# Kernel tuning notes

Measured on AMD Instinct MI355X. Metric: run time of the kernel, lower is better.

Reference implementation:

```python
import jax, jax.numpy as jnp
import numpy as np

A, M, H = 4, 1024, 1024
E, N = 8, 4096

def setup_inputs() -> dict:
    key = jax.random.key(0)
    kx, k1, k2 = jax.random.split(key, 3)
    x = jax.random.normal(kx, (A, M, H), dtype=jnp.float32)
    w1 = jax.random.normal(k1, (E, H, N), dtype=jnp.float32) * 0.02
    w2 = jax.random.normal(k2, (E, N, H), dtype=jnp.float32) * 0.02
    return {"x": x, "w1": w1, "w2": w2}

def reference(x, w1, w2):
    # mid: [A, E, M, N] = up-projection per expert
    mid = jnp.einsum('amh,ehn->aemn', x, w1)
    # down-projection per expert, then sum over experts e
    out = jnp.einsum('aemn,enh->amh', mid, w2)
    return out
```

## Files before the change

### kernel.cpp

```cpp
#include <hip/hip_runtime.h>
#include <hip/hip_bf16.h>
#include <stdint.h>


#define BN 128

typedef __attribute__((ext_vector_type(8))) short short8;
typedef __attribute__((ext_vector_type(4))) float float4v;
typedef __attribute__((ext_vector_type(4))) unsigned int uint4v;

__device__ __forceinline__ unsigned int rne_hi(unsigned int u) {
  return u + 0x7fffu + ((u >> 16) & 1u);
}

__device__ __forceinline__ unsigned int pack_bf16(float lo, float hi) {
  unsigned int ulo = rne_hi(__float_as_uint(lo));
  unsigned int uhi = rne_hi(__float_as_uint(hi));
  return __builtin_amdgcn_perm(uhi, ulo, 0x07060302u);
}

__device__ __forceinline__ void load_lds_16B(const void* g, void* lds) {
  __builtin_amdgcn_global_load_lds(
      (__attribute__((address_space(1))) void*)(uintptr_t)g,
      (__attribute__((address_space(3))) void*)(unsigned int)(uintptr_t)lds,
      16, 0, 0);
}

template <int MI, bool ATOMIC>
__global__ __launch_bounds__(256) void gemm_bf16(
    const unsigned short* __restrict__ A, int lda, long strideA,
    const unsigned short* __restrict__ Bt, int ldb, long strideB,
    float* __restrict__ C, int ldc, int K, int zdiv) {
  constexpr int BM = MI * 32;
  __shared__ __attribute__((aligned(16))) unsigned short As[2 * BM * 32];
  __shared__ __attribute__((aligned(16))) unsigned short Bs[2 * BN * 32];

  const int tid = threadIdx.x;
  const int wv = tid >> 6;
  const int ln = tid & 63;
  const int wm = (wv >> 1) * (MI * 16);
  const int wn = (wv & 1) * 64;
  const int lrow = ln & 15;
  const int lq = ln >> 4;
  const int sfrag = ((lq + (lrow >> 1)) & 3) * 16;

  const int zb = blockIdx.z / zdiv;
  const int zk = blockIdx.z % zdiv;
  const unsigned short* Ab = A + (long)zb * strideA + (long)zk * K +
                             (long)(blockIdx.y * BM) * lda;
  const unsigned short* Bb = Bt + (long)zb * strideB + (long)zk * K +
                             (long)(blockIdx.x * BN) * ldb;

  float4v zero4 = {0.0f, 0.0f, 0.0f, 0.0f};
  float4v acc[MI][4];
#pragma unroll
  for (int i = 0; i < MI; ++i)
#pragma unroll
    for (int j = 0; j < 4; ++j) acc[i][j] = zero4;

  const int nk = K / 64;
  for (int kt = 0; kt < nk; ++kt) {
    const int k0 = kt * 64;
    __syncthreads();
#pragma unroll
    for (int s = 0; s < 2; ++s) {
#pragma unroll
      for (int p = 0; p < BM / 64; ++p) {
        int o = p * 256 + wv * 64 + ln;
        int r = o >> 2;
        int gk = ((o & 3) - (r >> 1)) & 3;
        const unsigned short* g = Ab + (long)r * lda + k0 + s * 32 + gk * 8;
        char* lp = (char*)As + s * (BM * 64) + (p * 256 + wv * 64) * 16;
        load_lds_16B(g, lp);
      }
#pragma unroll
      for (int p = 0; p < 2; ++p) {
        int o = p * 256 + wv * 64 + ln;
        int r = o >> 2;
        int gk = ((o & 3) - (r >> 1)) & 3;
        const unsigned short* g = Bb + (long)r * ldb + k0 + s * 32 + gk * 8;
        char* lp = (char*)Bs + s * (BN * 64) + (p * 256 + wv * 64) * 16;
        load_lds_16B(g, lp);
      }
    }
    __syncthreads();

#pragma unroll
    for (int s = 0; s < 2; ++s) {
      short8 a[MI], b[4];
#pragma unroll
      for (int i = 0; i < MI; ++i)
        a[i] = *(const short8*)((const char*)As + s * (BM * 64) +
                                (wm + i * 16 + lrow) * 64 + sfrag);
#pragma unroll
      for (int j = 0; j < 4; ++j)
        b[j] = *(const short8*)((const char*)Bs + s * (BN * 64) +
                                (wn + j * 16 + lrow) * 64 + sfrag);
#pragma unroll
      for (int i = 0; i < MI; ++i)
#pragma unroll
        for (int j = 0; j < 4; ++j)
          acc[i][j] =
              __builtin_amdgcn_mfma_f32_16x16x32_bf16(a[i], b[j], acc[i][j], 0, 0, 0);
    }
  }

  const int crow0 = blockIdx.y * BM + wm + lq * 4;
  const int ccol0 = blockIdx.x * BN + wn + lrow;
#pragma unroll
  for (int i = 0; i < MI; ++i)
#pragma unroll
    for (int j = 0; j < 4; ++j)
#pragma unroll
      for (int r = 0; r < 4; ++r) {
        int row = crow0 + i * 16 + r;
        int col = ccol0 + j * 16;
        if (ATOMIC)
          atomicAdd(&C[(long)row * ldc + col], acc[i][j][r]);
        else
          C[(long)row * ldc + col] = acc[i][j][r];
      }
}

__global__ __launch_bounds__(256) void cvt_f32_bf16(
    const float* __restrict__ in, unsigned short* __restrict__ out) {
  long i = ((long)blockIdx.x * 256 + threadIdx.x) * 8;
  float4 v0 = *(const float4*)(in + i);
  float4 v1 = *(const float4*)(in + i + 4);
  uint4v d;
  d.x = pack_bf16(v0.x, v0.y);
  d.y = pack_bf16(v0.z, v0.w);
  d.z = pack_bf16(v1.x, v1.y);
  d.w = pack_bf16(v1.z, v1.w);
  *(uint4v*)(out + i) = d;
}

__global__ __launch_bounds__(256) void transpose_cvt_kernel(
    const float* __restrict__ in, unsigned short* __restrict__ out,
    int R, int C, long strideBatch) {
  __shared__ float tile[64][65];
  const float* src = in + (long)blockIdx.z * strideBatch;
  unsigned short* dst = out + (long)blockIdx.z * strideBatch;
  const int t = threadIdx.x;
  const int c4 = (t & 15) * 4;
  const int r0 = t >> 4;
  const int by = blockIdx.y * 64;
  const int bx = blockIdx.x * 64;
#pragma unroll
  for (int p = 0; p < 4; ++p) {
    int r = r0 + p * 16;
    float4 v = *(const float4*)(src + (long)(by + r) * C + bx + c4);
    tile[r][c4 + 0] = v.x;
    tile[r][c4 + 1] = v.y;
    tile[r][c4 + 2] = v.z;
    tile[r][c4 + 3] = v.w;
  }
  __syncthreads();
#pragma unroll
  for (int p = 0; p < 4; ++p) {
    int cc = r0 + p * 16;
    int rr = c4;
    unsigned int d0 = pack_bf16(tile[rr + 0][cc], tile[rr + 1][cc]);
    unsigned int d1 = pack_bf16(tile[rr + 2][cc], tile[rr + 3][cc]);
    uint2 dd;
    dd.x = d0;
    dd.y = d1;
    *(uint2*)(dst + (long)(bx + cc) * R + by + rr) = dd;
  }
}

extern "C" void kernel_launch(void* const* d_in, const int* in_sizes, int n_in,
                              void* d_out, int out_size, void* d_ws, size_t ws_size,
                              hipStream_t stream) {
  const float* x = (const float*)d_in[0];
  const float* w1 = (const float*)d_in[1];
  const float* w2 = (const float*)d_in[2];
  float* out = (float*)d_out;

  const int A_ = 4, M_ = 1024, H_ = 1024, E_ = 8, N_ = 4096;
  const long EXP = (long)H_ * N_;

  const size_t need_single =
      (size_t)2 * E_ * EXP * 2 + (size_t)A_ * M_ * H_ * 2 +
      (size_t)H_ * H_ * 4 + (size_t)H_ * H_ * 2;

  if (ws_size >= need_single) {
    unsigned short* w2t = (unsigned short*)d_ws;
    unsigned short* w1b = w2t + (long)E_ * EXP;
    unsigned short* xb = w1b + (long)E_ * EXP;
    float* Wacc = (float*)(xb + (long)A_ * M_ * H_);
    unsigned short* Wb = (unsigned short*)(Wacc + (long)H_ * H_);

    cvt_f32_bf16<<<(A_ * M_ * H_) / 2048, 256, 0, stream>>>(x, xb);
    transpose_cvt_kernel<<<dim3(H_ / 64, N_ / 64, E_), 256, 0, stream>>>(
        w2, w2t, N_, H_, EXP);
    cvt_f32_bf16<<<(int)(E_ * EXP / 2048), 256, 0, stream>>>(w1, w1b);
    hipMemsetAsync(Wacc, 0, (size_t)H_ * H_ * 4, stream);

    gemm_bf16<4, true><<<dim3(H_ / BN, H_ / 128, E_ * 2), 256, 0, stream>>>(
        w2t, N_, EXP, w1b, N_, EXP, Wacc, H_, N_ / 2, 2);

    cvt_f32_bf16<<<(H_ * H_) / 2048, 256, 0, stream>>>(Wacc, Wb);

    gemm_bf16<2, false><<<dim3(H_ / BN, (A_ * M_) / 64, 1), 256, 0, stream>>>(
        xb, H_, 0, Wb, H_, 0, out, H_, H_, 1);
  } else {
    unsigned short* w2t = (unsigned short*)d_ws;
    unsigned short* w1b = w2t + 4 * EXP;
    unsigned short* xb = w1b + 4 * EXP;
    float* Wacc = (float*)(xb + (long)A_ * M_ * H_);
    unsigned short* Wb = (unsigned short*)(Wacc + (long)H_ * H_);

    cvt_f32_bf16<<<(A_ * M_ * H_) / 2048, 256, 0, stream>>>(x, xb);
    hipMemsetAsync(Wacc, 0, (size_t)H_ * H_ * 4, stream);

    for (int g = 0; g < 2; ++g) {
      const float* w2g = w2 + (long)g * 4 * EXP;
      const float* w1g = w1 + (long)g * 4 * EXP;
      transpose_cvt_kernel<<<dim3(H_ / 64, N_ / 64, 4), 256, 0, stream>>>(
          w2g, w2t, N_, H_, EXP);
      cvt_f32_bf16<<<(int)(4 * EXP / 2048), 256, 0, stream>>>(w1g, w1b);
      gemm_bf16<4, true><<<dim3(H_ / BN, H_ / 128, 4 * 2), 256, 0, stream>>>(
          w2t, N_, EXP, w1b, N_, EXP, Wacc, H_, N_ / 2, 2);
    }

    cvt_f32_bf16<<<(H_ * H_) / 2048, 256, 0, stream>>>(Wacc, Wb);
    gemm_bf16<2, false><<<dim3(H_ / BN, (A_ * M_) / 64, 1), 256, 0, stream>>>(
        xb, H_, 0, Wb, H_, 0, out, H_, H_, 1);
  }
}
```

Measured before the change: 470.0 us.

## Replace weight-product GEMM with 256x256 tiled, 8-wave phased pipelined kernel

Adds a new GEMM for the W2^T·W1 weight-combination step. It uses 256x256 tiles with 512 threads, double-buffered LDS with an XOR swizzle, and a four-phase schedule per k-tile that interleaves global-to-LDS staging with MFMA groups run at raised wave priority. It also remaps workgroups across XCDs. The goal is to raise MFMA utilisation and data reuse over the old 128x128 kernel, at the cost of heavier register and LDS use and more barriers. In the fallback path the K split changes to 4 with grid 256.

```diff
diff --git a/kernel.cpp b/kernel.cpp
--- a/kernel.cpp
+++ b/kernel.cpp
@@ -24,6 +24,167 @@
       (__attribute__((address_space(1))) void*)(uintptr_t)g,
       (__attribute__((address_space(3))) void*)(unsigned int)(uintptr_t)lds,
       16, 0, 0);
+}
+
+
+template <int MH, int NH>
+__device__ __forceinline__ void mma_ph(float4v acc[8][4], const short8* aR,
+                                       const short8 bR[2][4]) {
+  __builtin_amdgcn_s_setprio(1);
+#pragma unroll
+  for (int fi = 0; fi < 4; ++fi)
+#pragma unroll
+    for (int fj = 0; fj < 2; ++fj)
+#pragma unroll
+      for (int s = 0; s < 2; ++s)
+        acc[MH * 4 + fi][NH * 2 + fj] = __builtin_amdgcn_mfma_f32_16x16x32_bf16(
+            aR[fi * 2 + s], bR[NH][fj * 2 + s], acc[MH * 4 + fi][NH * 2 + fj],
+            0, 0, 0);
+  __builtin_amdgcn_s_setprio(0);
+}
+
+__global__ __launch_bounds__(512, 2) void gemm1_8ph(
+    const unsigned short* __restrict__ A, const unsigned short* __restrict__ Bt,
+    float* __restrict__ C, long expStride, int ld, int Kc, int zdiv) {
+  __shared__ __attribute__((aligned(16))) unsigned short As[2][2][128 * 64];
+  __shared__ __attribute__((aligned(16))) unsigned short Bs[2][2][128 * 64];
+
+  const int tid = threadIdx.x;
+  const int wv = tid >> 6;
+  const int ln = tid & 63;
+  const int lrow = ln & 15;
+  const int lq = ln >> 4;
+  const int wmh = wv >> 2;
+  const int wnq = wv & 3;
+  const int breg = wnq >> 1;
+  const int brow0 = (wnq & 1) * 64;
+
+  const int nwg = gridDim.x;
+  int wg = blockIdx.x;
+  if ((nwg & 7) == 0) wg = (wg & 7) * (nwg >> 3) + (wg >> 3);
+  const int tile = wg & 15;
+  const int z = wg >> 4;
+  const int e = z / zdiv;
+  const int kc = z % zdiv;
+  const int ty = tile >> 2, tx = tile & 3;
+
+  const unsigned short* Ab =
+      A + (long)e * expStride + (long)(ty * 256) * ld + (long)kc * Kc;
+  const unsigned short* Bb =
+      Bt + (long)e * expStride + (long)(tx * 256) * ld + (long)kc * Kc;
+
+  const int srow = ln >> 3;
+  const int scg = (ln & 7) ^ srow;
+
+  auto stageA = [&](int b, int h, int kt) {
+#pragma unroll
+    for (int i = 0; i < 2; ++i) {
+      const unsigned short* g =
+          Ab + (long)(h * 128 + wv * 16 + i * 8 + srow) * ld + kt * 64 + scg * 8;
+      load_lds_16B(g, (void*)&As[b][h][(wv * 2 + i) * 512]);
+    }
+  };
+  auto stageB = [&](int b, int h, int kt) {
+#pragma unroll
+    for (int i = 0; i < 2; ++i) {
+      const unsigned short* g =
+          Bb + (long)(h * 128 + wv * 16 + i * 8 + srow) * ld + kt * 64 + scg * 8;
+      load_lds_16B(g, (void*)&Bs[b][h][(wv * 2 + i) * 512]);
+    }
+  };
+
+  float4v acc[8][4];
+  float4v zero4 = {0.0f, 0.0f, 0.0f, 0.0f};
+#pragma unroll
+  for (int i = 0; i < 8; ++i)
+#pragma unroll
+    for (int j = 0; j < 4; ++j) acc[i][j] = zero4;
+
+  short8 aR[8];
+  short8 bR[2][4];
+
+  auto ldsA = [&](int b, int mh) {
+#pragma unroll
+    for (int fi = 0; fi < 4; ++fi) {
+      const int row = mh * 64 + fi * 16 + lrow;
+#pragma unroll
+      for (int s = 0; s < 2; ++s) {
+        const int cg = (s * 4 + lq) ^ (row & 7);
+        aR[fi * 2 + s] = *(const short8*)&As[b][wmh][row * 64 + cg * 8];
+      }
+    }
+  };
+  auto ldsB = [&](int b, int nh) {
+#pragma unroll
+    for (int fj = 0; fj < 2; ++fj) {
+      const int row = brow0 + nh * 32 + fj * 16 + lrow;
+#pragma unroll
+      for (int s = 0; s < 2; ++s) {
+        const int cg = (s * 4 + lq) ^ (row & 7);
+        bR[nh][fj * 2 + s] = *(const short8*)&Bs[b][breg][row * 64 + cg * 8];
+      }
+    }
+  };
+
+  const int nkt = Kc / 64;
+
+  stageA(0, 0, 0);
+  stageA(0, 1, 0);
+  stageB(0, 0, 0);
+  stageB(0, 1, 0);
+  stageB(1, 0, 1);
+  stageB(1, 1, 1);
+  asm volatile("s_waitcnt vmcnt(4)" ::: "memory");
+  __builtin_amdgcn_s_barrier();
+
+#define HALF_ITER(B, OB, NN)                                        \
+  {                                                                 \
+    const int na = ((NN) + 1 < nkt) ? (NN) + 1 : nkt - 1;           \
+    const int nb = ((NN) + 2 < nkt) ? (NN) + 2 : nkt - 1;           \
+    ldsA(B, 0);                                                     \
+    ldsB(B, 0);                                                     \
+    stageA(OB, 0, na);                                              \
+    __builtin_amdgcn_s_barrier();                                   \
+    asm volatile("s_waitcnt lgkmcnt(0)");                           \
+    mma_ph<0, 0>(acc, aR, bR);                                      \
+    __builtin_amdgcn_s_barrier();                                   \
+    ldsB(B, 1);                                                     \
+    stageA(OB, 1, na);                                              \
+    __builtin_amdgcn_s_barrier();                                   \
+    asm volatile("s_waitcnt lgkmcnt(0)");                           \
+    mma_ph<0, 1>(acc, aR, bR);                                      \
+    __builtin_amdgcn_s_barrier();                                   \
+    ldsA(B, 1);                                                     \
+    stageB(B, 0, nb);                                               \
+    __builtin_amdgcn_s_barrier();                                   \
+    asm volatile("s_waitcnt lgkmcnt(0)");                           \
+    mma_ph<1, 1>(acc, aR, bR);                                      \
+    __builtin_amdgcn_s_barrier();                                   \
+    stageB(B, 1, nb);                                               \
+    __builtin_amdgcn_s_barrier();                                   \
+    mma_ph<1, 0>(acc, aR, bR);                                      \
+    asm volatile("s_waitcnt vmcnt(4)" ::: "memory");                \
+    __builtin_amdgcn_s_barrier();                                   \
+  }
+
+  for (int t = 0; t < nkt; t += 2) {
+    HALF_ITER(0, 1, t)
+    HALF_ITER(1, 0, t + 1)
+  }
+#undef HALF_ITER
+
+  asm volatile("s_waitcnt vmcnt(0)" ::: "memory");
+
+  const int crow0 = ty * 256 + wmh * 128 + lq * 4;
+  const int ccol0 = tx * 256 + wnq * 64 + lrow;
+#pragma unroll
+  for (int i = 0; i < 8; ++i)
+#pragma unroll
+    for (int j = 0; j < 4; ++j)
+#pragma unroll
+      for (int r = 0; r < 4; ++r)
+        atomicAdd(&C[(long)(crow0 + i * 16 + r) * 1024 + ccol0 + j * 16],
+                  acc[i][j][r]);
 }
 
 template <int MI, bool ATOMIC>
@@ -100,8 +261,8 @@
       for (int i = 0; i < MI; ++i)
 #pragma unroll
         for (int j = 0; j < 4; ++j)
-          acc[i][j] =
-              __builtin_amdgcn_mfma_f32_16x16x32_bf16(a[i], b[j], acc[i][j], 0, 0, 0);
+          acc[i][j] = __builtin_amdgcn_mfma_f32_16x16x32_bf16(a[i], b[j],
+                                                              acc[i][j], 0, 0, 0);
     }
   }
 
@@ -197,8 +358,7 @@
     cvt_f32_bf16<<<(int)(E_ * EXP / 2048), 256, 0, stream>>>(w1, w1b);
     hipMemsetAsync(Wacc, 0, (size_t)H_ * H_ * 4, stream);
 
-    gemm_bf16<4, true><<<dim3(H_ / BN, H_ / 128, E_ * 2), 256, 0, stream>>>(
-        w2t, N_, EXP, w1b, N_, EXP, Wacc, H_, N_ / 2, 2);
+    gemm1_8ph<<<dim3(256), 512, 0, stream>>>(w2t, w1b, Wacc, EXP, N_, N_ / 2, 2);
 
     cvt_f32_bf16<<<(H_ * H_) / 2048, 256, 0, stream>>>(Wacc, Wb);
 
@@ -220,8 +380,7 @@
       transpose_cvt_kernel<<<dim3(H_ / 64, N_ / 64, 4), 256, 0, stream>>>(
           w2g, w2t, N_, H_, EXP);
       cvt_f32_bf16<<<(int)(4 * EXP / 2048), 256, 0, stream>>>(w1g, w1b);
-      gemm_bf16<4, true><<<dim3(H_ / BN, H_ / 128, 4 * 2), 256, 0, stream>>>(
-          w2t, N_, EXP, w1b, N_, EXP, Wacc, H_, N_ / 2, 2);
+      gemm1_8ph<<<dim3(256), 512, 0, stream>>>(w2t, w1b, Wacc, EXP, N_, N_ / 4, 4);
     }
 
     cvt_f32_bf16<<<(H_ * H_) / 2048, 256, 0, stream>>>(Wacc, Wb);
```

Result: faster. 427.2 us (-9.1%).
